# Kernel tuning notes

Hardware: AMD Instinct MI355X
Metric: run time of the kernel (lower is better)

The kernel has to match this reference:

```python
import jax, jax.numpy as jnp
import numpy as np

F_DIM = 1024
HEAD = 16
MLP_H = 4096
EPS = 1e-5


def _layernorm(x, g, b):
    mu = jnp.mean(x, axis=-1, keepdims=True)
    var = jnp.var(x, axis=-1, keepdims=True)
    return (x - mu) * jax.lax.rsqrt(var + EPS) * g + b


def setup_inputs() -> dict:
    key = jax.random.key(0)
    ks = jax.random.split(key, 16)
    B, T, F = 2, 2048, F_DIM
    s = 1.0 / np.sqrt(F)
    sm = 1.0 / np.sqrt(MLP_H)
    return {
        "x": jax.random.normal(ks[0], (B, T, F), jnp.float32),
        "ln1_g": jnp.ones((F,), jnp.float32),
        "ln1_b": jnp.zeros((F,), jnp.float32),
        "Wq": jax.random.normal(ks[1], (F, F), jnp.float32) * s,
        "bq": jnp.zeros((F,), jnp.float32),
        "Wk": jax.random.normal(ks[2], (F, F), jnp.float32) * s,
        "bk": jnp.zeros((F,), jnp.float32),
        "Wv": jax.random.normal(ks[3], (F, F), jnp.float32) * s,
        "bv": jnp.zeros((F,), jnp.float32),
        "Wo": jax.random.normal(ks[4], (F, F), jnp.float32) * s,
        "bo": jnp.zeros((F,), jnp.float32),
        "ln2_g": jnp.ones((F,), jnp.float32),
        "ln2_b": jnp.zeros((F,), jnp.float32),
        "W1": jax.random.normal(ks[5], (F, MLP_H), jnp.float32) * s,
        "b1": jnp.zeros((MLP_H,), jnp.float32),
        "W2": jax.random.normal(ks[6], (MLP_H, F), jnp.float32) * sm,
        "b2": jnp.zeros((F,), jnp.float32),
    }


def reference(x, ln1_g, ln1_b, Wq, bq, Wk, bk, Wv, bv, Wo, bo, ln2_g, ln2_b, W1, b1, W2, b2):
    B, T, F = x.shape
    H, Dh = HEAD, F // HEAD
    sqrt_d = jnp.asarray(F, x.dtype) ** 0.5  # NOTE: scale by sqrt(features), as in source

    h = _layernorm(x, ln1_g, ln1_b)
    Q = (h @ Wq + bq).reshape(B, T, H, Dh).transpose(0, 2, 1, 3)  # bhtd
    K = (h @ Wk + bk).reshape(B, T, H, Dh).transpose(0, 2, 1, 3)
    V = (h @ Wv + bv).reshape(B, T, H, Dh).transpose(0, 2, 1, 3)

    scores = jnp.einsum('bhif,bhjf->bhij', Q, K) / sqrt_d
    attn_map = jax.nn.softmax(scores, axis=-1)
    attn = jnp.einsum('bhij,bhjf->bihf', attn_map, V)  # [B,T,H,Dh]
    attn_out = attn.reshape(B, T, F) @ Wo + bo
    out = attn_out + x

    h2 = _layernorm(out, ln2_g, ln2_b)
    mlp = jax.nn.gelu(jax.nn.gelu(h2 @ W1 + b1, approximate=False) @ W2 + b2, approximate=False)
    return mlp + out
```

## Files before the change

kernel.cpp:

```cpp
#include <hip/hip_runtime.h>
#include <hip/hip_bf16.h>
#include <math.h>
#include <stdint.h>

typedef __attribute__((ext_vector_type(8))) __bf16 bf16x8;
typedef __attribute__((ext_vector_type(4))) float f32x4;

#define F_DIM 1024
#define MLP_HD 4096
#define HEADS 16
#define DH 64
#define B_SZ 2
#define T_SZ 2048
#define NROWS 4096
#define QKV_N 3072
#define LN_EPS 1e-5f

__device__ __forceinline__ void gload16(const void* g, void* l) {
    __builtin_amdgcn_global_load_lds(
        (const __attribute__((address_space(1))) uint32_t*)(uintptr_t)g,
        (__attribute__((address_space(3))) uint32_t*)(uintptr_t)l,
        16, 0, 0);
}

__global__ void transpose_cast4(const float* __restrict__ s0, const float* __restrict__ s1,
                                const float* __restrict__ s2, const float* __restrict__ s3,
                                __hip_bfloat16* __restrict__ d0, __hip_bfloat16* __restrict__ d1,
                                __hip_bfloat16* __restrict__ d2, __hip_bfloat16* __restrict__ d3) {
    __shared__ float tile[32][33];
    const float* in = blockIdx.z == 0 ? s0 : blockIdx.z == 1 ? s1 : blockIdx.z == 2 ? s2 : s3;
    __hip_bfloat16* out = blockIdx.z == 0 ? d0 : blockIdx.z == 1 ? d1 : blockIdx.z == 2 ? d2 : d3;
    int c0 = blockIdx.x * 32, r0 = blockIdx.y * 32;
    int tx = threadIdx.x, ty = threadIdx.y;
    #pragma unroll
    for (int i = 0; i < 32; i += 8)
        tile[ty + i][tx] = in[(size_t)(r0 + ty + i) * 1024 + c0 + tx];
    __syncthreads();
    #pragma unroll
    for (int i = 0; i < 32; i += 8)
        out[(size_t)(c0 + ty + i) * 1024 + r0 + tx] = __float2bfloat16(tile[tx][ty + i]);
}

__global__ void transpose_cast(const float* __restrict__ in,
                               __hip_bfloat16* __restrict__ out,
                               int R, int C) {
    __shared__ float tile[32][33];
    int c0 = blockIdx.x * 32, r0 = blockIdx.y * 32;
    int tx = threadIdx.x, ty = threadIdx.y;
    #pragma unroll
    for (int i = 0; i < 32; i += 8)
        tile[ty + i][tx] = in[(size_t)(r0 + ty + i) * C + c0 + tx];
    __syncthreads();
    #pragma unroll
    for (int i = 0; i < 32; i += 8)
        out[(size_t)(c0 + ty + i) * R + r0 + tx] = __float2bfloat16(tile[tx][ty + i]);
}

__global__ void transpose_v(const __hip_bfloat16* __restrict__ QKV,
                            __hip_bfloat16* __restrict__ VT) {
    __shared__ __hip_bfloat16 tile[32][33];
    int dblk = blockIdx.y & 1, bh = blockIdx.y >> 1;
    int b = bh >> 4, h = bh & 15;
    int t0 = blockIdx.x * 32, d0 = dblk * 32;
    int tx = threadIdx.x, ty = threadIdx.y;
    #pragma unroll
    for (int i = 0; i < 32; i += 8)
        tile[ty + i][tx] = QKV[(size_t)(b * T_SZ + t0 + ty + i) * QKV_N + 2048 + h * DH + d0 + tx];
    __syncthreads();
    #pragma unroll
    for (int i = 0; i < 32; i += 8)
        VT[(size_t)(bh * DH + d0 + ty + i) * T_SZ + t0 + tx] = tile[tx][ty + i];
}

__global__ void concat_bias(const float* __restrict__ a, const float* __restrict__ b,
                            const float* __restrict__ c, float* __restrict__ o) {
    int i = blockIdx.x * 256 + threadIdx.x;
    o[i] = i < 1024 ? a[i] : (i < 2048 ? b[i - 1024] : c[i - 2048]);
}

__global__ void layernorm_bf16_k(const float* __restrict__ x,
                                 const float* __restrict__ g,
                                 const float* __restrict__ b,
                                 __hip_bfloat16* __restrict__ out) {
    int row = blockIdx.x;
    const float* xr = x + (size_t)row * F_DIM;
    int t = threadIdx.x;
    float4 v = ((const float4*)xr)[t];
    float s  = v.x + v.y + v.z + v.w;
    float s2 = v.x * v.x + v.y * v.y + v.z * v.z + v.w * v.w;
    #pragma unroll
    for (int off = 32; off >= 1; off >>= 1) {
        s  += __shfl_down(s, off);
        s2 += __shfl_down(s2, off);
    }
    __shared__ float rs_[4], rs2_[4];
    int wave = t >> 6, lane = t & 63;
    if (lane == 0) { rs_[wave] = s; rs2_[wave] = s2; }
    __syncthreads();
    float S  = rs_[0] + rs_[1] + rs_[2] + rs_[3];
    float S2 = rs2_[0] + rs2_[1] + rs2_[2] + rs2_[3];
    float mu  = S * (1.0f / F_DIM);
    float var = S2 * (1.0f / F_DIM) - mu * mu;
    float rstd = rsqrtf(var + LN_EPS);
    float4 gv = ((const float4*)g)[t];
    float4 bv = ((const float4*)b)[t];
    __hip_bfloat16* orow = out + (size_t)row * F_DIM;
    orow[t * 4 + 0] = __float2bfloat16((v.x - mu) * rstd * gv.x + bv.x);
    orow[t * 4 + 1] = __float2bfloat16((v.y - mu) * rstd * gv.y + bv.y);
    orow[t * 4 + 2] = __float2bfloat16((v.z - mu) * rstd * gv.z + bv.z);
    orow[t * 4 + 3] = __float2bfloat16((v.w - mu) * rstd * gv.w + bv.w);
}

__device__ __forceinline__ float gelu_fast(float x) {
    float u = 0.7978845608f * (x + 0.044715f * x * x * x);
    u = fminf(fmaxf(u, -10.f), 10.f);
    float e = __expf(2.0f * u);
    float th = (e - 1.0f) / (e + 1.0f);
    return 0.5f * x * (1.0f + th);
}

#define LA_PTR(BUF, H) ((__hip_bfloat16*)(SMEM + ((BUF) * 2 + (H)) * 16384))
#define LB_PTR(BUF, H) ((__hip_bfloat16*)(SMEM + 65536 + ((BUF) * 2 + (H)) * 16384))

#define MFMA_QUAD(AF, BF, MB, NB)                                              \
  do {                                                                         \
    __builtin_amdgcn_s_barrier();                                              \
    asm volatile("s_waitcnt lgkmcnt(0)" ::: "memory");                         \
    __builtin_amdgcn_sched_barrier(0);                                         \
    __builtin_amdgcn_s_setprio(1);                                             \
    _Pragma("unroll") for (int ks = 0; ks < 2; ++ks)                           \
      _Pragma("unroll") for (int a_ = 0; a_ < 4; ++a_)                         \
        _Pragma("unroll") for (int b_ = 0; b_ < 2; ++b_)                       \
          acc[(MB) + a_][(NB) + b_] = __builtin_amdgcn_mfma_f32_16x16x32_bf16( \
              AF[a_][ks], BF[b_][ks], acc[(MB) + a_][(NB) + b_], 0, 0, 0);     \
    __builtin_amdgcn_s_setprio(0);                                             \
  } while (0)

#define LDA_FRAGS(DST, BUF, MQ)                                                \
  do {                                                                         \
    _Pragma("unroll") for (int a_ = 0; a_ < 4; ++a_)                           \
      _Pragma("unroll") for (int ks = 0; ks < 2; ++ks) {                       \
        int row_ = (MQ) * 64 + a_ * 16 + fr;                                   \
        int byt_ = row_ * 128 + ((ks * 64 + fq * 16) ^ ((row_ & 7) << 4));     \
        DST[a_][ks] = *(const bf16x8*)((const char*)LA_PTR(BUF, wm) + byt_);   \
      }                                                                        \
  } while (0)

#define LDB_FRAGS(DST, BUF, NQ)                                                \
  do {                                                                         \
    _Pragma("unroll") for (int b_ = 0; b_ < 2; ++b_)                           \
      _Pragma("unroll") for (int ks = 0; ks < 2; ++ks) {                       \
        int row_ = (wn & 1) * 64 + ((NQ) * 2 + b_) * 16 + fr;                  \
        int byt_ = row_ * 128 + ((ks * 64 + fq * 16) ^ ((row_ & 7) << 4));     \
        DST[b_][ks] = *(const bf16x8*)((const char*)LB_PTR(BUF, hb) + byt_);   \
      }                                                                        \
  } while (0)

#define STAGE_A(BUF, H, KT_)                                                   \
  do {                                                                         \
    _Pragma("unroll") for (int q_ = 0; q_ < 2; ++q_)                           \
      gload16(A + (size_t)(m0 + (H) * 128 + srow[q_]) * K +                    \
                  (k00 + (KT_) * 64 + scol[q_]),                               \
              LA_PTR(BUF, H) + q_ * 4096 + t * 8);                             \
  } while (0)

#define STAGE_B(BUF, H, KT_)                                                   \
  do {                                                                         \
    _Pragma("unroll") for (int q_ = 0; q_ < 2; ++q_)                           \
      gload16(BT + (size_t)(n0 + (H) * 128 + srow[q_]) * K +                   \
                   (k00 + (KT_) * 64 + scol[q_]),                              \
              LB_PTR(BUF, H) + q_ * 4096 + t * 8);                             \
  } while (0)

template <int EPI, int KLEN>
__global__ __launch_bounds__(512, 2) void gemm256(
    const __hip_bfloat16* __restrict__ A,
    const __hip_bfloat16* __restrict__ BT,
    const float* __restrict__ bias,
    void* __restrict__ Cout,
    int M, int N, int K) {
    __shared__ __align__(16) char SMEM[131072];

    int t = threadIdx.x;
    int w = t >> 6, lane = t & 63;
    int wm = w >> 2, wn = w & 3;
    int fr = lane & 15, fq = lane >> 4;
    int hb = wn >> 1;

    int gx = gridDim.x, gy = gridDim.y, gz = gridDim.z;
    int bid = blockIdx.x + gx * (blockIdx.y + gy * blockIdx.z);
    int nwg = gx * gy * gz;
    int qch = nwg >> 3;
    int logical = (bid & 7) * qch + (bid >> 3);
    int pp = gy * gz;
    int bx = logical / pp;
    int rr = logical % pp;
    int by = rr / gz;
    int bz = rr % gz;

    int m0 = by * 256, n0 = bx * 256;
    int k00 = bz * KLEN;

    int srow[2], scol[2];
    #pragma unroll
    for (int q = 0; q < 2; ++q) {
        int u = q * 8192 + t * 16;
        u ^= ((u >> 7) & 7) << 4;
        srow[q] = u >> 7;
        scol[q] = (u & 127) >> 1;
    }

    f32x4 acc[8][4] = {};
    bf16x8 aflo[4][2], afhi[4][2], bflo[2][2], bfhi[2][2];
    constexpr int KT = KLEN >> 6;

    STAGE_A(0, 0, 0); STAGE_A(0, 1, 0); STAGE_B(0, 0, 0); STAGE_B(0, 1, 0);
    STAGE_A(1, 0, 1); STAGE_A(1, 1, 1);
    asm volatile("s_waitcnt vmcnt(4)" ::: "memory");
    __builtin_amdgcn_s_barrier();

    for (int i = 0;; ++i) {
        int k1 = 2 * i + 1;
        int nx2 = (2 * i + 2) & (KT - 1), nx3 = (2 * i + 3) & (KT - 1);
        LDA_FRAGS(aflo, 0, 0);
        LDB_FRAGS(bflo, 0, 0);
        STAGE_B(1, 0, k1);
        MFMA_QUAD(aflo, bflo, 0, 0);
        __builtin_amdgcn_s_barrier();
        LDA_FRAGS(afhi, 0, 1);
        STAGE_B(1, 1, k1);
        MFMA_QUAD(afhi, bflo, 4, 0);
        __builtin_amdgcn_s_barrier();
        LDB_FRAGS(bfhi, 0, 1);
        STAGE_A(0, 0, nx2);
        MFMA_QUAD(afhi, bfhi, 4, 2);
        __builtin_amdgcn_s_barrier();
        STAGE_A(0, 1, nx2);
        MFMA_QUAD(aflo, bfhi, 0, 2);
        asm volatile("s_waitcnt vmcnt(4)" ::: "memory");
        __builtin_amdgcn_s_barrier();
        LDA_FRAGS(aflo, 1, 0);
        LDB_FRAGS(bflo, 1, 0);
        STAGE_B(0, 0, nx2);
        MFMA_QUAD(aflo, bflo, 0, 0);
        __builtin_amdgcn_s_barrier();
        LDA_FRAGS(afhi, 1, 1);
        STAGE_B(0, 1, nx2);
        MFMA_QUAD(afhi, bflo, 4, 0);
        __builtin_amdgcn_s_barrier();
        LDB_FRAGS(bfhi, 1, 1);
        STAGE_A(1, 0, nx3);
        MFMA_QUAD(afhi, bfhi, 4, 2);
        __builtin_amdgcn_s_barrier();
        STAGE_A(1, 1, nx3);
        MFMA_QUAD(aflo, bfhi, 0, 2);
        asm volatile("s_waitcnt vmcnt(4)" ::: "memory");
        __builtin_amdgcn_s_barrier();
        if (2 * i + 2 >= KT) break;
    }

    asm volatile("s_waitcnt vmcnt(0)" ::: "memory");
    __builtin_amdgcn_s_barrier();

    #pragma unroll
    for (int ni = 0; ni < 4; ++ni) {
        int col = wn * 64 + ni * 16 + fr;
        float bv = (EPI == 4) ? 0.f : bias[n0 + col];
        #pragma unroll
        for (int mi = 0; mi < 8; ++mi) {
            #pragma unroll
            for (int j = 0; j < 4; ++j) {
                int row = wm * 128 + mi * 16 + fq * 4 + j;
                float v = acc[mi][ni][j] + bv;
                if constexpr (EPI == 2) v = gelu_fast(v);
                int byt = row * 512 + ((col * 2) ^ ((row & 7) << 4));
                *(__hip_bfloat16*)(SMEM + byt) = __float2bfloat16(v);
            }
        }
    }
    __builtin_amdgcn_s_barrier();

    __hip_bfloat16* outc = (__hip_bfloat16*)Cout;
    if constexpr (EPI == 4) outc += (size_t)bz * ((size_t)M * N);
    #pragma unroll
    for (int p = 0; p < 16; ++p) {
        int row = p * 16 + (t >> 5);
        int chunk = t & 31;
        int byt = row * 512 + ((chunk * 16) ^ ((row & 7) << 4));
        bf16x8 vv = *(const bf16x8*)(SMEM + byt);
        *(bf16x8*)&outc[(size_t)(m0 + row) * N + n0 + chunk * 8] = vv;
    }
}

__global__ __launch_bounds__(256) void mlp2_reduce(
    const __hip_bfloat16* __restrict__ P,
    const float* __restrict__ b2,
    const float* __restrict__ res,
    float* __restrict__ out) {
    int i = (blockIdx.x * 256 + threadIdx.x) * 8;
    float s[8] = {};
    #pragma unroll
    for (int sk = 0; sk < 4; ++sk) {
        bf16x8 v = *(const bf16x8*)&P[(size_t)sk * ((size_t)NROWS * F_DIM) + i];
        #pragma unroll
        for (int u = 0; u < 8; ++u) s[u] += (float)v[u];
    }
    int col = i & (F_DIM - 1);
    #pragma unroll
    for (int u = 0; u < 8; ++u)
        out[i + u] = gelu_fast(s[u] + b2[col + u]) + res[i + u];
}

template <int EPI, int BM>
__global__ __launch_bounds__(256) void gemm_bt(
    const __hip_bfloat16* __restrict__ A,
    const __hip_bfloat16* __restrict__ BT,
    const float* __restrict__ bias,
    const float* __restrict__ res,
    void* __restrict__ Cout,
    int M, int N, int K) {
    constexpr int MI = BM / 32;
    constexpr int AQ = BM / 64;
    __shared__ __hip_bfloat16 As[2][BM * 32];
    __shared__ __hip_bfloat16 Bs[2][128 * 32];

    int t = threadIdx.x;
    int m0 = blockIdx.y * BM, n0 = blockIdx.x * 128;
    int w = t >> 6, lane = t & 63;
    int wr = (w >> 1) * (BM / 2), wc = (w & 1) * 64;
    int fr = lane & 15, fq = lane >> 4;

    int scol = (lane & 3) * 8;
    int srowA = w * (BM / 4) + (lane >> 2);
    int srowB = w * 32 + (lane >> 2);
    const __hip_bfloat16* Ag = A  + (size_t)(m0 + srowA) * K + scol;
    const __hip_bfloat16* Bg = BT + (size_t)(n0 + srowB) * K + scol;
    int lofsA = w * (BM / 4) * 32 + lane * 8;
    int lofsB = w * 1024 + lane * 8;

    f32x4 acc[MI][4] = {};
    int KT = K >> 5;
    int cur = 0;

    #pragma unroll
    for (int q = 0; q < AQ; ++q)
        gload16(Ag + (size_t)q * 16 * K, &As[0][lofsA + q * 512]);
    #pragma unroll
    for (int q = 0; q < 2; ++q)
        gload16(Bg + (size_t)q * 16 * K, &Bs[0][lofsB + q * 512]);
    __syncthreads();

    for (int kt = 0; kt < KT; ++kt) {
        if (kt + 1 < KT) {
            const __hip_bfloat16* An = Ag + (size_t)(kt + 1) * 32;
            const __hip_bfloat16* Bn = Bg + (size_t)(kt + 1) * 32;
            #pragma unroll
            for (int q = 0; q < AQ; ++q)
                gload16(An + (size_t)q * 16 * K, &As[cur ^ 1][lofsA + q * 512]);
            #pragma unroll
            for (int q = 0; q < 2; ++q)
                gload16(Bn + (size_t)q * 16 * K, &Bs[cur ^ 1][lofsB + q * 512]);
        }
        bf16x8 af[MI], bfr[4];
        #pragma unroll
        for (int mi = 0; mi < MI; ++mi)
            af[mi] = *(const bf16x8*)&As[cur][(wr + mi * 16 + fr) * 32 + fq * 8];
        #pragma unroll
        for (int ni = 0; ni < 4; ++ni)
            bfr[ni] = *(const bf16x8*)&Bs[cur][(wc + ni * 16 + fr) * 32 + fq * 8];
        #pragma unroll
        for (int mi = 0; mi < MI; ++mi)
            #pragma unroll
            for (int ni = 0; ni < 4; ++ni)
                acc[mi][ni] = __builtin_amdgcn_mfma_f32_16x16x32_bf16(
                    af[mi], bfr[ni], acc[mi][ni], 0, 0, 0);
        __syncthreads();
        cur ^= 1;
    }

    #pragma unroll
    for (int ni = 0; ni < 4; ++ni) {
        int col = n0 + wc + ni * 16 + fr;
        float bv = bias[col];
        #pragma unroll
        for (int mi = 0; mi < MI; ++mi) {
            #pragma unroll
            for (int j = 0; j < 4; ++j) {
                int row = m0 + wr + mi * 16 + fq * 4 + j;
                size_t idx = (size_t)row * N + col;
                float v = acc[mi][ni][j] + bv;
                if constexpr (EPI == 1) {
                    ((float*)Cout)[idx] = v + res[idx];
                } else {
                    ((__hip_bfloat16*)Cout)[idx] = __float2bfloat16(v);
                }
            }
        }
    }
}

#define KVB 32
#define NT2 (T_SZ / KVB)

__global__ __launch_bounds__(256, 4) void attn_mfma(
    const __hip_bfloat16* __restrict__ QKV,
    const __hip_bfloat16* __restrict__ VT,
    __hip_bfloat16* __restrict__ O) {
    __shared__ __hip_bfloat16 Kt[2][KVB][72];
    __shared__ __hip_bfloat16 Vt[2][DH][44];
    __shared__ __hip_bfloat16 Ps[4][32][40];

    int hw = blockIdx.x;
    int blk = (hw & 7) * 64 + (hw >> 3);
    int qb = blk & 15;
    int bh = blk >> 4;
    int b = bh >> 4, h = bh & 15;
    int t = threadIdx.x;
    int w = t >> 6, lane = t & 63;
    int fr = lane & 15, fq = lane >> 4;

    bf16x8 qf[2][2];
    #pragma unroll
    for (int mt = 0; mt < 2; ++mt)
        #pragma unroll
        for (int ks = 0; ks < 2; ++ks) {
            int qrow = qb * 128 + w * 32 + mt * 16 + fr;
            const __hip_bfloat16* src =
                QKV + (size_t)(b * T_SZ + qrow) * QKV_N + h * DH + ks * 32 + fq * 8;
            bf16x8 v = *(const bf16x8*)src;
            #pragma unroll
            for (int u = 0; u < 8; ++u) v[u] = (__bf16)((float)v[u] * 0.03125f);
            qf[mt][ks] = v;
        }

    f32x4 oacc[2][4] = {};
    float lsum[2][4] = {};

    int krow = t >> 3, kcol = (t & 7) * 8;
    int vrow = t >> 2, vcol = (t & 3) * 8;
    const __hip_bfloat16* Kg = QKV + (size_t)(b * T_SZ + krow) * QKV_N + F_DIM + h * DH + kcol;
    const __hip_bfloat16* Vg = VT + (size_t)(bh * DH + vrow) * T_SZ + vcol;

    bf16x8 kr, vr;
    kr = *(const bf16x8*)Kg;
    vr = *(const bf16x8*)Vg;
    *(bf16x8*)&Kt[0][krow][kcol] = kr;
    *(bf16x8*)&Vt[0][vrow][vcol] = vr;
    kr = *(const bf16x8*)(Kg + (size_t)KVB * QKV_N);
    vr = *(const bf16x8*)(Vg + KVB);
    __syncthreads();

    #pragma unroll 2
    for (int i = 0; i < NT2; ++i) {
        int cur = i & 1;
        if (i + 1 < NT2) {
            *(bf16x8*)&Kt[cur ^ 1][krow][kcol] = kr;
            *(bf16x8*)&Vt[cur ^ 1][vrow][vcol] = vr;
        }
        if (i + 2 < NT2) {
            kr = *(const bf16x8*)(Kg + (size_t)(i + 2) * KVB * QKV_N);
            vr = *(const bf16x8*)(Vg + (i + 2) * KVB);
        }

        f32x4 sacc[2][2];
        __builtin_amdgcn_s_setprio(1);
        {
            bf16x8 kf[2][2];
            #pragma unroll
            for (int nt = 0; nt < 2; ++nt)
                #pragma unroll
                for (int ks = 0; ks < 2; ++ks)
                    kf[nt][ks] = *(const bf16x8*)&Kt[cur][nt * 16 + fr][ks * 32 + fq * 8];
            #pragma unroll
            for (int mt = 0; mt < 2; ++mt)
                #pragma unroll
                for (int nt = 0; nt < 2; ++nt) {
                    f32x4 zz = {0.f, 0.f, 0.f, 0.f};
                    f32x4 s0 = __builtin_amdgcn_mfma_f32_16x16x32_bf16(
                        qf[mt][0], kf[nt][0], zz, 0, 0, 0);
                    sacc[mt][nt] = __builtin_amdgcn_mfma_f32_16x16x32_bf16(
                        qf[mt][1], kf[nt][1], s0, 0, 0, 0);
                }
        }
        __builtin_amdgcn_s_setprio(0);

        #pragma unroll
        for (int mt = 0; mt < 2; ++mt)
            #pragma unroll
            for (int r = 0; r < 4; ++r)
                #pragma unroll
                for (int nt = 0; nt < 2; ++nt) {
                    float p = __expf(sacc[mt][nt][r]);
                    lsum[mt][r] += p;
                    Ps[w][mt * 16 + fq * 4 + r][nt * 16 + fr] = __float2bfloat16(p);
                }

        asm volatile("s_waitcnt lgkmcnt(0)" ::: "memory");
        __builtin_amdgcn_sched_barrier(0);

        __builtin_amdgcn_s_setprio(1);
        {
            bf16x8 ap[2];
            #pragma unroll
            for (int mt = 0; mt < 2; ++mt)
                ap[mt] = *(const bf16x8*)&Ps[w][mt * 16 + fr][fq * 8];
            #pragma unroll
            for (int nd = 0; nd < 4; ++nd) {
                bf16x8 vbv = *(const bf16x8*)&Vt[cur][nd * 16 + fr][fq * 8];
                #pragma unroll
                for (int mt = 0; mt < 2; ++mt)
                    oacc[mt][nd] = __builtin_amdgcn_mfma_f32_16x16x32_bf16(
                        ap[mt], vbv, oacc[mt][nd], 0, 0, 0);
            }
        }
        __builtin_amdgcn_s_setprio(0);

        __syncthreads();
    }

    #pragma unroll
    for (int mt = 0; mt < 2; ++mt) {
        #pragma unroll
        for (int r = 0; r < 4; ++r) {
            float l = lsum[mt][r];
            #pragma unroll
            for (int d = 1; d < 16; d <<= 1) l += __shfl_xor(l, d);
            float rl = 1.0f / l;
            int row = qb * 128 + w * 32 + mt * 16 + fq * 4 + r;
            #pragma unroll
            for (int nt = 0; nt < 4; ++nt)
                O[(size_t)(b * T_SZ + row) * F_DIM + h * DH + nt * 16 + fr] =
                    __float2bfloat16(oacc[mt][nt][r] * rl);
        }
    }
}

extern "C" void kernel_launch(void* const* d_in, const int* in_sizes, int n_in,
                              void* d_out, int out_size, void* d_ws, size_t ws_size,
                              hipStream_t stream) {
    const float* x     = (const float*)d_in[0];
    const float* ln1_g = (const float*)d_in[1];
    const float* ln1_b = (const float*)d_in[2];
    const float* Wq    = (const float*)d_in[3];
    const float* bq    = (const float*)d_in[4];
    const float* Wk    = (const float*)d_in[5];
    const float* bk    = (const float*)d_in[6];
    const float* Wv    = (const float*)d_in[7];
    const float* bv    = (const float*)d_in[8];
    const float* Wo    = (const float*)d_in[9];
    const float* bo    = (const float*)d_in[10];
    const float* ln2_g = (const float*)d_in[11];
    const float* ln2_b = (const float*)d_in[12];
    const float* W1    = (const float*)d_in[13];
    const float* b1    = (const float*)d_in[14];
    const float* W2    = (const float*)d_in[15];
    const float* b2    = (const float*)d_in[16];
    float* outp = (float*)d_out;

    char* ws = (char*)d_ws;
    size_t off = 0;
    auto alloc = [&](size_t bytes) {
        void* p = ws + off;
        off += (bytes + 255) & ~(size_t)255;
        return p;
    };
    __hip_bfloat16* WqkvT = (__hip_bfloat16*)alloc((size_t)QKV_N * 1024 * 2);
    __hip_bfloat16* WoT   = (__hip_bfloat16*)alloc((size_t)1024 * 1024 * 2);
    __hip_bfloat16* W1T   = (__hip_bfloat16*)alloc((size_t)4096 * 1024 * 2);
    __hip_bfloat16* W2T   = (__hip_bfloat16*)alloc((size_t)4096 * 1024 * 2);
    float*          qkvb  = (float*)alloc((size_t)QKV_N * 4);
    __hip_bfloat16* h1    = (__hip_bfloat16*)alloc((size_t)NROWS * F_DIM * 2);
    __hip_bfloat16* QKVb  = (__hip_bfloat16*)alloc((size_t)NROWS * QKV_N * 2);
    __hip_bfloat16* VTb   = (__hip_bfloat16*)alloc((size_t)32 * DH * T_SZ * 2);
    __hip_bfloat16* attnO = (__hip_bfloat16*)alloc((size_t)NROWS * F_DIM * 2);
    float*          outb  = (float*)alloc((size_t)NROWS * F_DIM * 4);
    __hip_bfloat16* h2    = (__hip_bfloat16*)alloc((size_t)NROWS * F_DIM * 2);
    __hip_bfloat16* mlp1  = (__hip_bfloat16*)alloc((size_t)NROWS * MLP_HD * 2);
    __hip_bfloat16* mlp2P = h1;
    (void)ws_size; (void)in_sizes; (void)n_in; (void)out_size;

    dim3 tb(32, 8);
    transpose_cast4<<<dim3(32, 32, 4), tb, 0, stream>>>(
        Wq, Wk, Wv, Wo,
        WqkvT, WqkvT + 1024 * 1024, WqkvT + 2048 * 1024, WoT);
    transpose_cast<<<dim3(128, 32), tb, 0, stream>>>(W1, W1T, 1024, 4096);
    transpose_cast<<<dim3(32, 128), tb, 0, stream>>>(W2, W2T, 4096, 1024);
    concat_bias<<<12, 256, 0, stream>>>(bq, bk, bv, qkvb);

    layernorm_bf16_k<<<NROWS, 256, 0, stream>>>(x, ln1_g, ln1_b, h1);

    gemm256<0, 1024><<<dim3(QKV_N / 256, NROWS / 256, 1), 512, 0, stream>>>(
        h1, WqkvT, qkvb, QKVb, NROWS, QKV_N, 1024);

    transpose_v<<<dim3(T_SZ / 32, 64), tb, 0, stream>>>(QKVb, VTb);

    attn_mfma<<<512, 256, 0, stream>>>(QKVb, VTb, attnO);

    gemm_bt<1, 64><<<dim3(8, 64), 256, 0, stream>>>(attnO, WoT, bo, x, outb, NROWS, 1024, 1024);

    layernorm_bf16_k<<<NROWS, 256, 0, stream>>>(outb, ln2_g, ln2_b, h2);

    gemm256<2, 1024><<<dim3(MLP_HD / 256, NROWS / 256, 1), 512, 0, stream>>>(
        h2, W1T, b1, mlp1, NROWS, MLP_HD, 1024);

    gemm256<4, 1024><<<dim3(F_DIM / 256, NROWS / 256, 4), 512, 0, stream>>>(
        mlp1, W2T, nullptr, mlp2P, NROWS, F_DIM, MLP_HD);

    mlp2_reduce<<<2048, 256, 0, stream>>>(mlp2P, b2, outb, outp);
}
```

Measured before the change: 236.2 us.

## Compute transposed attention scores and pass P through lane shuffles instead of LDS

The attention kernel now computes S^T (K as the A operand, Q as B) so each lane holds one query column, then packs exp(S) into bf16 pairs and rearranges them with cross-lane shuffles into the B-operand layout for the PV MFMA. This removes the per-wave LDS staging buffer for P along with its waitcnt/sched barrier. The output is computed transposed, so each lane writes 4 contiguous bf16 values and the row-sum reduction shrinks to two shuffles. The cost is 16 shuffles plus selects per tile in place of LDS writes and reads.

```diff
diff --git a/kernel.cpp b/kernel.cpp
--- a/kernel.cpp
+++ b/kernel.cpp
@@ -4,6 +4,7 @@
 #include <stdint.h>
 
 typedef __attribute__((ext_vector_type(8))) __bf16 bf16x8;
+typedef __attribute__((ext_vector_type(4))) __bf16 bf16x4;
 typedef __attribute__((ext_vector_type(4))) float f32x4;
 
 #define F_DIM 1024
@@ -402,13 +403,18 @@
 #define KVB 32
 #define NT2 (T_SZ / KVB)
 
+__device__ __forceinline__ unsigned pkbf16(float a, float b) {
+    union { __bf16 h[2]; unsigned u; } x;
+    x.h[0] = (__bf16)a; x.h[1] = (__bf16)b;
+    return x.u;
+}
+
 __global__ __launch_bounds__(256, 4) void attn_mfma(
     const __hip_bfloat16* __restrict__ QKV,
     const __hip_bfloat16* __restrict__ VT,
     __hip_bfloat16* __restrict__ O) {
     __shared__ __hip_bfloat16 Kt[2][KVB][72];
     __shared__ __hip_bfloat16 Vt[2][DH][44];
-    __shared__ __hip_bfloat16 Ps[4][32][40];
 
     int hw = blockIdx.x;
     int blk = (hw & 7) * 64 + (hw >> 3);
@@ -421,20 +427,20 @@
 
     bf16x8 qf[2][2];
     #pragma unroll
-    for (int mt = 0; mt < 2; ++mt)
+    for (int qt = 0; qt < 2; ++qt)
         #pragma unroll
         for (int ks = 0; ks < 2; ++ks) {
-            int qrow = qb * 128 + w * 32 + mt * 16 + fr;
+            int qrow = qb * 128 + w * 32 + qt * 16 + fr;
             const __hip_bfloat16* src =
                 QKV + (size_t)(b * T_SZ + qrow) * QKV_N + h * DH + ks * 32 + fq * 8;
             bf16x8 v = *(const bf16x8*)src;
             #pragma unroll
             for (int u = 0; u < 8; ++u) v[u] = (__bf16)((float)v[u] * 0.03125f);
-            qf[mt][ks] = v;
+            qf[qt][ks] = v;
         }
 
     f32x4 oacc[2][4] = {};
-    float lsum[2][4] = {};
+    float lsum[2] = {0.f, 0.f};
 
     int krow = t >> 3, kcol = (t & 7) * 8;
     int vrow = t >> 2, vcol = (t & 3) * 8;
@@ -450,6 +456,10 @@
     vr = *(const bf16x8*)(Vg + KVB);
     __syncthreads();
 
+    int s0 = ((lane & 16) << 1) | (lane & 15);
+    int s1 = s0 + 16;
+    bool hilane = lane >= 32;
+
     #pragma unroll 2
     for (int i = 0; i < NT2; ++i) {
         int cur = i & 1;
@@ -462,56 +472,58 @@
             vr = *(const bf16x8*)(Vg + (i + 2) * KVB);
         }
 
-        f32x4 sacc[2][2];
+        f32x4 st[2][2];
         __builtin_amdgcn_s_setprio(1);
         {
             bf16x8 kf[2][2];
             #pragma unroll
-            for (int nt = 0; nt < 2; ++nt)
+            for (int jt = 0; jt < 2; ++jt)
                 #pragma unroll
                 for (int ks = 0; ks < 2; ++ks)
-                    kf[nt][ks] = *(const bf16x8*)&Kt[cur][nt * 16 + fr][ks * 32 + fq * 8];
-            #pragma unroll
-            for (int mt = 0; mt < 2; ++mt)
+                    kf[jt][ks] = *(const bf16x8*)&Kt[cur][jt * 16 + fr][ks * 32 + fq * 8];
+            #pragma unroll
+            for (int qt = 0; qt < 2; ++qt)
                 #pragma unroll
-                for (int nt = 0; nt < 2; ++nt) {
+                for (int jt = 0; jt < 2; ++jt) {
                     f32x4 zz = {0.f, 0.f, 0.f, 0.f};
-                    f32x4 s0 = __builtin_amdgcn_mfma_f32_16x16x32_bf16(
-                        qf[mt][0], kf[nt][0], zz, 0, 0, 0);
-                    sacc[mt][nt] = __builtin_amdgcn_mfma_f32_16x16x32_bf16(
-                        qf[mt][1], kf[nt][1], s0, 0, 0, 0);
+                    f32x4 p0 = __builtin_amdgcn_mfma_f32_16x16x32_bf16(
+                        kf[jt][0], qf[qt][0], zz, 0, 0, 0);
+                    st[qt][jt] = __builtin_amdgcn_mfma_f32_16x16x32_bf16(
+                        kf[jt][1], qf[qt][1], p0, 0, 0, 0);
                 }
         }
         __builtin_amdgcn_s_setprio(0);
 
-        #pragma unroll
-        for (int mt = 0; mt < 2; ++mt)
-            #pragma unroll
-            for (int r = 0; r < 4; ++r)
-                #pragma unroll
-                for (int nt = 0; nt < 2; ++nt) {
-                    float p = __expf(sacc[mt][nt][r]);
-                    lsum[mt][r] += p;
-                    Ps[w][mt * 16 + fq * 4 + r][nt * 16 + fr] = __float2bfloat16(p);
-                }
-
-        asm volatile("s_waitcnt lgkmcnt(0)" ::: "memory");
-        __builtin_amdgcn_sched_barrier(0);
+        bf16x8 pb[2];
+        #pragma unroll
+        for (int qt = 0; qt < 2; ++qt) {
+            float p00 = __expf(st[qt][0][0]), p01 = __expf(st[qt][0][1]);
+            float p02 = __expf(st[qt][0][2]), p03 = __expf(st[qt][0][3]);
+            float p10 = __expf(st[qt][1][0]), p11 = __expf(st[qt][1][1]);
+            float p12 = __expf(st[qt][1][2]), p13 = __expf(st[qt][1][3]);
+            lsum[qt] += ((p00 + p01) + (p02 + p03)) + ((p10 + p11) + (p12 + p13));
+            unsigned L0 = pkbf16(p00, p01), L1 = pkbf16(p02, p03);
+            unsigned H0 = pkbf16(p10, p11), H1 = pkbf16(p12, p13);
+            unsigned a0 = (unsigned)__shfl((int)L0, s0), b0 = (unsigned)__shfl((int)H0, s0);
+            unsigned a1 = (unsigned)__shfl((int)L1, s0), b1 = (unsigned)__shfl((int)H1, s0);
+            unsigned a2 = (unsigned)__shfl((int)L0, s1), b2 = (unsigned)__shfl((int)H0, s1);
+            unsigned a3 = (unsigned)__shfl((int)L1, s1), b3 = (unsigned)__shfl((int)H1, s1);
+            union { unsigned wds[4]; bf16x8 v; } U;
+            U.wds[0] = hilane ? b0 : a0;
+            U.wds[1] = hilane ? b1 : a1;
+            U.wds[2] = hilane ? b2 : a2;
+            U.wds[3] = hilane ? b3 : a3;
+            pb[qt] = U.v;
+        }
 
         __builtin_amdgcn_s_setprio(1);
-        {
-            bf16x8 ap[2];
-            #pragma unroll
-            for (int mt = 0; mt < 2; ++mt)
-                ap[mt] = *(const bf16x8*)&Ps[w][mt * 16 + fr][fq * 8];
-            #pragma unroll
-            for (int nd = 0; nd < 4; ++nd) {
-                bf16x8 vbv = *(const bf16x8*)&Vt[cur][nd * 16 + fr][fq * 8];
-                #pragma unroll
-                for (int mt = 0; mt < 2; ++mt)
-                    oacc[mt][nd] = __builtin_amdgcn_mfma_f32_16x16x32_bf16(
-                        ap[mt], vbv, oacc[mt][nd], 0, 0, 0);
-            }
+        #pragma unroll
+        for (int dt = 0; dt < 4; ++dt) {
+            bf16x8 vf = *(const bf16x8*)&Vt[cur][dt * 16 + fr][fq * 8];
+            oacc[0][dt] = __builtin_amdgcn_mfma_f32_16x16x32_bf16(
+                vf, pb[0], oacc[0][dt], 0, 0, 0);
+            oacc[1][dt] = __builtin_amdgcn_mfma_f32_16x16x32_bf16(
+                vf, pb[1], oacc[1][dt], 0, 0, 0);
         }
         __builtin_amdgcn_s_setprio(0);
 
@@ -519,18 +531,19 @@
     }
 
     #pragma unroll
-    for (int mt = 0; mt < 2; ++mt) {
-        #pragma unroll
-        for (int r = 0; r < 4; ++r) {
-            float l = lsum[mt][r];
-            #pragma unroll
-            for (int d = 1; d < 16; d <<= 1) l += __shfl_xor(l, d);
-            float rl = 1.0f / l;
-            int row = qb * 128 + w * 32 + mt * 16 + fq * 4 + r;
-            #pragma unroll
-            for (int nt = 0; nt < 4; ++nt)
-                O[(size_t)(b * T_SZ + row) * F_DIM + h * DH + nt * 16 + fr] =
-                    __float2bfloat16(oacc[mt][nt][r] * rl);
+    for (int qt = 0; qt < 2; ++qt) {
+        float l = lsum[qt];
+        l += __shfl_xor(l, 16);
+        l += __shfl_xor(l, 32);
+        float rl = 1.0f / l;
+        int qrow = qb * 128 + w * 32 + qt * 16 + fr;
+        __hip_bfloat16* orow = O + (size_t)(b * T_SZ + qrow) * F_DIM + h * DH;
+        #pragma unroll
+        for (int dt = 0; dt < 4; ++dt) {
+            bf16x4 ov;
+            #pragma unroll
+            for (int r = 0; r < 4; ++r) ov[r] = (__bf16)(oacc[qt][dt][r] * rl);
+            *(bf16x4*)&orow[dt * 16 + fq * 4] = ov;
         }
     }
 }
```

Result: slower. 244.3 us (+3.4%).
